# Kernel tuning notes

Hardware: AMD Instinct MI355X
Metric: run time of the kernel (lower is better)

## Reference

```python
import jax, jax.numpy as jnp
import numpy as np

NH = 12   # num_heads
EPS = 1e-6


def _layer_norm(x):
    m = jnp.mean(x, axis=-1, keepdims=True)
    v = jnp.mean((x - m) ** 2, axis=-1, keepdims=True)
    return (x - m) * jax.lax.rsqrt(v + EPS)


def _rms_norm(x, w):
    return x * jax.lax.rsqrt(jnp.mean(x * x, axis=-1, keepdims=True) + EPS) * w


def _rope_cos_sin(f, h, w, head_dim):
    # matches rope_params + calculate_freqs_i: split c=head_dim//2 complex freqs
    # into [c-2*(c//3), c//3, c//3] for the (F,H,W) axes.
    c = head_dim // 2
    inv = 1.0 / (10000.0 ** (np.arange(0, head_dim, 2, dtype=np.float64) / head_dim))
    c1 = c - 2 * (c // 3); c2 = c // 3
    af = np.outer(np.arange(f), inv[:c1])
    ah = np.outer(np.arange(h), inv[c1:c1 + c2])
    aw = np.outer(np.arange(w), inv[c1 + c2:])
    ang = np.concatenate([
        np.broadcast_to(af[:, None, None, :], (f, h, w, c1)),
        np.broadcast_to(ah[None, :, None, :], (f, h, w, c2)),
        np.broadcast_to(aw[None, None, :, :], (f, h, w, c2)),
    ], axis=-1).reshape(f * h * w, c)
    return jnp.asarray(np.cos(ang), jnp.float32), jnp.asarray(np.sin(ang), jnp.float32)


def _apply_rope(x, cos, sin):
    # complex rotation on interleaved pairs; x: [B,L,n,d]
    B, L, n, d = x.shape
    xr = x.reshape(B, L, n, d // 2, 2)
    x0, x1 = xr[..., 0], xr[..., 1]
    co = cos[None, :, None, :]; si = sin[None, :, None, :]
    return jnp.stack([x0 * co - x1 * si, x0 * si + x1 * co], axis=-1).reshape(B, L, n, d)


def _attention(q, k, v):
    scale = 1.0 / jnp.sqrt(jnp.asarray(q.shape[-1], q.dtype))
    s = jnp.einsum('blnd,bmnd->bnlm', q, k) * scale
    return jnp.einsum('bnlm,bmnd->blnd', jax.nn.softmax(s, axis=-1), v)


def _block(x, e, context, mod, sa_wq, sa_bq, sa_wk, sa_bk, sa_wv, sa_bv, sa_wo, sa_bo,
           sa_nq, sa_nk, n3_w, n3_b, ca_wq, ca_bq, ca_wk, ca_bk, ca_wv, ca_bv, ca_wo,
           ca_bo, ca_nq, ca_nk, ffn_w1, ffn_b1, ffn_w2, ffn_b2, f, h, w):
    B, L, C = x.shape
    D = C // NH
    em = mod + e                      # [B,6,C] AdaLN shift/scale/gate params
    cos, sin = _rope_cos_sin(f, h, w, D)
    # --- self-attention with AdaLN modulation + RoPE + qk RMSNorm ---
    xa = _layer_norm(x) * (1.0 + em[:, 1:2]) + em[:, 0:1]
    q = _rms_norm(xa @ sa_wq + sa_bq, sa_nq).reshape(B, L, NH, D)
    k = _rms_norm(xa @ sa_wk + sa_bk, sa_nk).reshape(B, L, NH, D)
    v = (xa @ sa_wv + sa_bv).reshape(B, L, NH, D)
    q = _apply_rope(q, cos, sin)
    k = _apply_rope(k, cos, sin)
    y = _attention(q, k, v).reshape(B, L, C) @ sa_wo + sa_bo
    x = x + y * em[:, 2:3]
    # --- t2v cross-attention (norm3 is affine LayerNorm) ---
    L2 = context.shape[1]
    xc = _layer_norm(x) * n3_w + n3_b
    q = _rms_norm(xc @ ca_wq + ca_bq, ca_nq).reshape(B, L, NH, D)
    k = _rms_norm(context @ ca_wk + ca_bk, ca_nk).reshape(B, L2, NH, D)
    v = (context @ ca_wv + ca_bv).reshape(B, L2, NH, D)
    x = x + (_attention(q, k, v).reshape(B, L, C) @ ca_wo + ca_bo)
    # --- FFN (GELU-tanh) with AdaLN modulation ---
    xf = _layer_norm(x) * (1.0 + em[:, 4:5]) + em[:, 3:4]
    y = jax.nn.gelu(xf @ ffn_w1 + ffn_b1, approximate=True) @ ffn_w2 + ffn_b2
    return x + y * em[:, 5:6]


def setup_inputs() -> dict:
    key = jax.random.key(0)
    ks = jax.random.split(key, 16)
    B, L2, C, FFN = 1, 512, 1536, 8960
    F, H, W = 9, 16, 28
    L = F * H * W  # 4032
    def mk(i, shape, s=0.02):
        return jax.random.normal(ks[i], shape, jnp.float32) * s
    return {
        'x': jax.random.normal(ks[0], (B, L, C), jnp.float32),
        'e': jax.random.normal(ks[1], (B, 6, C), jnp.float32),
        'context': jax.random.normal(ks[2], (B, L2, C), jnp.float32),
        'mod': jax.random.normal(ks[3], (1, 6, C), jnp.float32) / jnp.sqrt(float(C)),
        'sa_wq': mk(4, (C, C)), 'sa_bq': jnp.zeros((C,), jnp.float32),
        'sa_wk': mk(5, (C, C)), 'sa_bk': jnp.zeros((C,), jnp.float32),
        'sa_wv': mk(6, (C, C)), 'sa_bv': jnp.zeros((C,), jnp.float32),
        'sa_wo': mk(7, (C, C)), 'sa_bo': jnp.zeros((C,), jnp.float32),
        'sa_nq': jnp.ones((C,), jnp.float32), 'sa_nk': jnp.ones((C,), jnp.float32),
        'n3_w': jnp.ones((C,), jnp.float32), 'n3_b': jnp.zeros((C,), jnp.float32),
        'ca_wq': mk(8, (C, C)), 'ca_bq': jnp.zeros((C,), jnp.float32),
        'ca_wk': mk(9, (C, C)), 'ca_bk': jnp.zeros((C,), jnp.float32),
        'ca_wv': mk(10, (C, C)), 'ca_bv': jnp.zeros((C,), jnp.float32),
        'ca_wo': mk(11, (C, C)), 'ca_bo': jnp.zeros((C,), jnp.float32),
        'ca_nq': jnp.ones((C,), jnp.float32), 'ca_nk': jnp.ones((C,), jnp.float32),
        'ffn_w1': mk(12, (C, FFN)), 'ffn_b1': jnp.zeros((FFN,), jnp.float32),
        'ffn_w2': mk(13, (FFN, C)), 'ffn_b2': jnp.zeros((C,), jnp.float32),
        'f': F, 'h': H, 'w': W,
    }


def reference(x, e, context, mod, sa_wq, sa_bq, sa_wk, sa_bk, sa_wv, sa_bv, sa_wo,
              sa_bo, sa_nq, sa_nk, n3_w, n3_b, ca_wq, ca_bq, ca_wk, ca_bk, ca_wv,
              ca_bv, ca_wo, ca_bo, ca_nq, ca_nk, ffn_w1, ffn_b1, ffn_w2, ffn_b2,
              f, h, w):
    return _block(x, e, context, mod, sa_wq, sa_bq, sa_wk, sa_bk, sa_wv, sa_bv,
                  sa_wo, sa_bo, sa_nq, sa_nk, n3_w, n3_b, ca_wq, ca_bq, ca_wk,
                  ca_bk, ca_wv, ca_bv, ca_wo, ca_bo, ca_nq, ca_nk, ffn_w1, ffn_b1,
                  ffn_w2, ffn_b2, f, h, w)
```

## Files before the change

kernel.cpp:

```cpp
#include <hip/hip_runtime.h>
#include <math.h>


#define L_SEQ 4032
#define L_PAD 4096
#define C_DIM 1536
#define L_CTX 512
#define FFN_DIM 8960
#define NHEAD 12
#define DHEAD 128

typedef __attribute__((ext_vector_type(8))) short short8;
typedef __attribute__((ext_vector_type(4))) float floatx4;

__device__ inline unsigned short f2bf(float x) {
  unsigned int u = __float_as_uint(x);
  u += 0x7fffu + ((u >> 16) & 1u);
  return (unsigned short)(u >> 16);
}

__device__ inline float2 block_sum2(float2 v) {
  __shared__ float2 red[4];
#pragma unroll
  for (int o = 32; o > 0; o >>= 1) {
    v.x += __shfl_xor(v.x, o, 64);
    v.y += __shfl_xor(v.y, o, 64);
  }
  int wave = threadIdx.x >> 6;
  if ((threadIdx.x & 63) == 0) red[wave] = v;
  __syncthreads();
  float2 t = make_float2(0.f, 0.f);
#pragma unroll
  for (int i = 0; i < 4; ++i) { t.x += red[i].x; t.y += red[i].y; }
  return t;
}

__global__ void add_kernel(float* __restrict__ o, const float* __restrict__ a,
                           const float* __restrict__ b, int n) {
  int i = blockIdx.x * 256 + threadIdx.x;
  if (i < n) o[i] = a[i] + b[i];
}

__global__ void concat3_kernel(float* __restrict__ o, const float* __restrict__ a,
                               const float* __restrict__ b, const float* __restrict__ c) {
  int i = blockIdx.x * 256 + threadIdx.x;
  if (i < C_DIM) {
    o[i] = a[i];
    o[C_DIM + i] = b[i];
    if (c) o[2 * C_DIM + i] = c[i];
  }
}

__global__ void f32_to_bf16_kernel(unsigned short* __restrict__ o,
                                   const float* __restrict__ in, int n) {
  int i = (blockIdx.x * 256 + threadIdx.x) * 4;
  if (i < n) {
    float4 v = *(const float4*)&in[i];
    ushort4 o4 = {f2bf(v.x), f2bf(v.y), f2bf(v.z), f2bf(v.w)};
    *(ushort4*)&o[i] = o4;
  }
}

__global__ __launch_bounds__(256) void transpose_bf16_kernel(
    const float* __restrict__ W, unsigned short* __restrict__ WT, int K, int N) {
  __shared__ float t[32][33];
  int n0 = blockIdx.x * 32, k0 = blockIdx.y * 32;
  int c = threadIdx.x & 31, r0 = threadIdx.x >> 5;
#pragma unroll
  for (int i = 0; i < 4; ++i) {
    int r = r0 + 8 * i;
    t[r][c] = W[(size_t)(k0 + r) * N + n0 + c];
  }
  __syncthreads();
#pragma unroll
  for (int i = 0; i < 4; ++i) {
    int r = r0 + 8 * i;
    WT[(size_t)(n0 + r) * K + k0 + c] = f2bf(t[c][r]);
  }
}

__global__ __launch_bounds__(256) void transpose_v_kernel(
    const float* __restrict__ V, unsigned short* __restrict__ Vt, int stride, int Lk) {
  __shared__ float t[32][33];
  int k0 = blockIdx.x * 32, c0 = blockIdx.y * 32;
  int c = threadIdx.x & 31, r0 = threadIdx.x >> 5;
#pragma unroll
  for (int i = 0; i < 4; ++i) {
    int r = r0 + 8 * i;
    t[r][c] = V[(size_t)(k0 + r) * stride + c0 + c];
  }
  __syncthreads();
#pragma unroll
  for (int i = 0; i < 4; ++i) {
    int r = r0 + 8 * i;
    Vt[(size_t)(c0 + r) * Lk + k0 + c] = f2bf(t[c][r]);
  }
}

__global__ __launch_bounds__(256) void ln_affine_kernel(
    unsigned short* __restrict__ out, const float* __restrict__ in,
    const float* __restrict__ sc, const float* __restrict__ sh, float addOne) {
  int row = blockIdx.x;
  const float* xr = in + (size_t)row * C_DIM;
  float vals[C_DIM / 256];
  float2 p = make_float2(0.f, 0.f);
  int cnt = 0;
  for (int c = threadIdx.x; c < C_DIM; c += 256) {
    float v = xr[c];
    vals[cnt++] = v;
    p.x += v; p.y += v * v;
  }
  float2 t = block_sum2(p);
  float mean = t.x * (1.f / C_DIM);
  float var = t.y * (1.f / C_DIM) - mean * mean;
  float r = rsqrtf(var + 1e-6f);
  cnt = 0;
  for (int c = threadIdx.x; c < C_DIM; c += 256) {
    float xh = (vals[cnt++] - mean) * r;
    out[(size_t)row * C_DIM + c] = f2bf(xh * (addOne + sc[c]) + sh[c]);
  }
}

template <int ROPE>
__global__ __launch_bounds__(256) void rms_post_kernel(
    unsigned short* __restrict__ obf, const float* __restrict__ in,
    const float* __restrict__ w, const float* __restrict__ cosb,
    const float* __restrict__ sinb, int stride) {
  int row = blockIdx.x;
  const float* xr = in + (size_t)row * stride;
  int c0 = threadIdx.x * 6;
  float v[6];
  *(float2*)&v[0] = *(const float2*)&xr[c0];
  *(float2*)&v[2] = *(const float2*)&xr[c0 + 2];
  *(float2*)&v[4] = *(const float2*)&xr[c0 + 4];
  float s2 = 0.f;
#pragma unroll
  for (int i = 0; i < 6; ++i) s2 += v[i] * v[i];
  float2 t = block_sum2(make_float2(s2, 0.f));
  float r = rsqrtf(t.x * (1.f / C_DIM) + 1e-6f);
#pragma unroll
  for (int i = 0; i < 6; ++i) v[i] *= r * w[c0 + i];
  if (ROPE) {
#pragma unroll
    for (int i = 0; i < 3; ++i) {
      int c = c0 + 2 * i;
      int j = (c & 127) >> 1;
      float co = cosb[row * 64 + j], si = sinb[row * 64 + j];
      float a = v[2 * i], b = v[2 * i + 1];
      v[2 * i] = a * co - b * si;
      v[2 * i + 1] = a * si + b * co;
    }
  }
  unsigned short* op = obf + (size_t)row * C_DIM + c0;
  ushort2 o01 = {f2bf(v[0]), f2bf(v[1])};
  ushort2 o23 = {f2bf(v[2]), f2bf(v[3])};
  ushort2 o45 = {f2bf(v[4]), f2bf(v[5])};
  *(ushort2*)&op[0] = o01;
  *(ushort2*)&op[2] = o23;
  *(ushort2*)&op[4] = o45;
}

__global__ void rope_tables_kernel(float* __restrict__ cosb, float* __restrict__ sinb) {
  int l = blockIdx.x, j = threadIdx.x;
  int f = l / (16 * 28);
  int rem = l % (16 * 28);
  int hh = rem / 28, ww = rem % 28;
  double inv = pow(10000.0, -(double)(2 * j) / 128.0);
  double pos = (j < 22) ? (double)f : ((j < 43) ? (double)hh : (double)ww);
  double ang = pos * inv;
  cosb[l * 64 + j] = (float)cos(ang);
  sinb[l * 64 + j] = (float)sin(ang);
}

__device__ inline float gelu_tanh(float x) {
  float x3 = x * x * x;
  return 0.5f * x * (1.f + tanhf(0.79788456080286535588f * (x + 0.044715f * x3)));
}

template <int EPI>
__global__ __launch_bounds__(256) void mgemm_kernel(
    const unsigned short* __restrict__ A, const unsigned short* __restrict__ BT,
    const float* __restrict__ bias, void* __restrict__ Cout,
    const float* __restrict__ resid, const float* __restrict__ gate,
    int N, int K, int Mlimit) {
  __shared__ short sA[2][4096];
  __shared__ short sB[2][4096];
  const int tid = threadIdx.x;
  const int wv = tid >> 6, lane = tid & 63;
  const int lm = lane & 15, lq = lane >> 4;
  const int wr = wv >> 1, wc = wv & 1;

  const int gx = gridDim.x;
  const int nwg = gx * gridDim.y;
  int flat = blockIdx.y * gx + blockIdx.x;
  {
    int qq = nwg >> 3, rr = nwg & 7;
    int xcd = flat & 7, idx = flat >> 3;
    flat = (xcd < rr ? xcd * (qq + 1) : rr * (qq + 1) + (xcd - rr) * qq) + idx;
  }
  const int row0 = (flat / gx) * 128, col0 = (flat % gx) * 128;

  floatx4 zero4 = {0.f, 0.f, 0.f, 0.f};
  floatx4 acc[4][4];
#pragma unroll
  for (int i = 0; i < 4; ++i)
#pragma unroll
    for (int j = 0; j < 4; ++j) acc[i][j] = zero4;

  const unsigned short* Abase = A + ((size_t)row0 + lm) * K + lq * 8;
  const unsigned short* Bbase = BT + ((size_t)col0 + lm) * K + lq * 8;

  auto stage = [&](int buf, int k0) {
#pragma unroll
    for (int t = 0; t < 2; ++t) {
      int g = wv * 2 + t;
      __builtin_amdgcn_global_load_lds(
          (const __attribute__((address_space(1))) void*)(Abase + (size_t)(g * 16) * K + k0),
          (__attribute__((address_space(3))) void*)(sA[buf] + g * 512), 16, 0, 0);
      __builtin_amdgcn_global_load_lds(
          (const __attribute__((address_space(1))) void*)(Bbase + (size_t)(g * 16) * K + k0),
          (__attribute__((address_space(3))) void*)(sB[buf] + g * 512), 16, 0, 0);
    }
  };

  stage(0, 0);
  __syncthreads();
  int cur = 0;
  const int nk = K >> 5;
  for (int t = 0; t < nk; ++t) {
    if (t + 1 < nk) stage(cur ^ 1, (t + 1) << 5);
    const short* sAc = &sA[cur][0];
    const short* sBc = &sB[cur][0];
    short8 af[4], bfv[4];
#pragma unroll
    for (int mt = 0; mt < 4; ++mt)
      af[mt] = *(const short8*)(sAc + (wr * 4 + mt) * 512 + lane * 8);
#pragma unroll
    for (int nt = 0; nt < 4; ++nt)
      bfv[nt] = *(const short8*)(sBc + (wc * 4 + nt) * 512 + lane * 8);
#pragma unroll
    for (int mt = 0; mt < 4; ++mt)
#pragma unroll
      for (int nt = 0; nt < 4; ++nt)
        acc[mt][nt] = __builtin_amdgcn_mfma_f32_16x16x32_bf16(
            af[mt], bfv[nt], acc[mt][nt], 0, 0, 0);
    __syncthreads();
    cur ^= 1;
  }

#pragma unroll
  for (int nt = 0; nt < 4; ++nt) {
    int colg = col0 + wc * 64 + nt * 16 + lm;
    float bv = bias[colg];
    float gv = (EPI == 2 && gate) ? gate[colg] : 1.f;
#pragma unroll
    for (int mt = 0; mt < 4; ++mt) {
#pragma unroll
      for (int r = 0; r < 4; ++r) {
        int rowg = row0 + wr * 64 + mt * 16 + lq * 4 + r;
        if (rowg < Mlimit) {
          float v = acc[mt][nt][r] + bv;
          if (EPI == 1) {
            ((unsigned short*)Cout)[(size_t)rowg * N + colg] = f2bf(gelu_tanh(v));
          } else if (EPI == 2) {
            ((float*)Cout)[(size_t)rowg * N + colg] =
                resid[(size_t)rowg * N + colg] + v * gv;
          } else {
            ((float*)Cout)[(size_t)rowg * N + colg] = v;
          }
        }
      }
    }
  }
}

__global__ __launch_bounds__(256) void attn_mfma_kernel(
    const unsigned short* __restrict__ Qb, const unsigned short* __restrict__ Kb,
    const unsigned short* __restrict__ Vt, unsigned short* __restrict__ O,
    int Lk) {
  __shared__ short sK[2][4096];
  __shared__ short sV[2][4096];
  __shared__ short sP[4][512];
  const int h = blockIdx.y;
  const int q0 = blockIdx.x * 64;
  const int tid = threadIdx.x;
  const int wv = tid >> 6, lane = tid & 63;
  const int lm = lane & 15, lq = lane >> 4;
  const float scale2 = 0.12751649737103347f;

  short8 qf[4];
  {
    const unsigned short* qrow =
        Qb + (size_t)(q0 + wv * 16 + lm) * C_DIM + h * DHEAD + lq * 8;
#pragma unroll
    for (int dc = 0; dc < 4; ++dc) qf[dc] = *(const short8*)(qrow + dc * 32);
  }

  floatx4 zero4 = {0.f, 0.f, 0.f, 0.f};
  floatx4 acc[8];
#pragma unroll
  for (int g = 0; g < 8; ++g) acc[g] = zero4;
  float m[4], l[4];
#pragma unroll
  for (int r = 0; r < 4; ++r) { m[r] = -1e30f; l[r] = 0.f; }

  auto stageKV = [&](int buf, int k0) {
#pragma unroll
    for (int t = 0; t < 2; ++t) {
      int g = wv * 2 + t;
      int nt_ = g >> 2, dc = g & 3;
      const unsigned short* srck =
          Kb + (size_t)(k0 + nt_ * 16 + lm) * C_DIM + h * DHEAD + dc * 32 + lq * 8;
      __builtin_amdgcn_global_load_lds(
          (const __attribute__((address_space(1))) void*)srck,
          (__attribute__((address_space(3))) void*)(sK[buf] + g * 512), 16, 0, 0);
      const unsigned short* srcv =
          Vt + (size_t)(h * DHEAD + g * 16 + lm) * Lk + k0 + lq * 8;
      __builtin_amdgcn_global_load_lds(
          (const __attribute__((address_space(1))) void*)srcv,
          (__attribute__((address_space(3))) void*)(sV[buf] + g * 512), 16, 0, 0);
    }
  };

  stageKV(0, 0);
  __syncthreads();
  int cur = 0;
  const int nsteps = Lk >> 5;
  for (int t = 0; t < nsteps; ++t) {
    if (t + 1 < nsteps) stageKV(cur ^ 1, (t + 1) << 5);
    const short* sKc = &sK[cur][0];
    const short* sVc = &sV[cur][0];

    floatx4 s0 = zero4, s1 = zero4;
#pragma unroll
    for (int dc = 0; dc < 4; ++dc) {
      short8 kf0 = *(const short8*)(sKc + dc * 512 + lane * 8);
      short8 kf1 = *(const short8*)(sKc + (4 + dc) * 512 + lane * 8);
      s0 = __builtin_amdgcn_mfma_f32_16x16x32_bf16(qf[dc], kf0, s0, 0, 0, 0);
      s1 = __builtin_amdgcn_mfma_f32_16x16x32_bf16(qf[dc], kf1, s1, 0, 0, 0);
    }

    float e0[4], e1[4], pm[4];
    bool need = false;
#pragma unroll
    for (int r = 0; r < 4; ++r) {
      e0[r] = s0[r] * scale2;
      e1[r] = s1[r] * scale2;
      float mx = fmaxf(e0[r], e1[r]);
      mx = fmaxf(mx, __shfl_xor(mx, 1));
      mx = fmaxf(mx, __shfl_xor(mx, 2));
      mx = fmaxf(mx, __shfl_xor(mx, 4));
      mx = fmaxf(mx, __shfl_xor(mx, 8));
      pm[r] = mx;
      need = need || (mx > m[r] + 11.5f);
    }
    if (__any((int)need)) {
#pragma unroll
      for (int r = 0; r < 4; ++r) {
        float mn = fmaxf(m[r], pm[r]);
        float al = exp2f(m[r] - mn);
        m[r] = mn;
        l[r] *= al;
#pragma unroll
        for (int g = 0; g < 8; ++g) acc[g][r] *= al;
      }
    }
#pragma unroll
    for (int r = 0; r < 4; ++r) {
      float p0 = exp2f(e0[r] - m[r]);
      float p1 = exp2f(e1[r] - m[r]);
      float rs = p0 + p1;
      rs += __shfl_xor(rs, 1);
      rs += __shfl_xor(rs, 2);
      rs += __shfl_xor(rs, 4);
      rs += __shfl_xor(rs, 8);
      l[r] += rs;
      e0[r] = p0;
      e1[r] = p1;
    }
    {
      int base0 = ((lm >> 3) * 16 + lq * 4) * 8 + (lm & 7);
      int base1 = ((2 + (lm >> 3)) * 16 + lq * 4) * 8 + (lm & 7);
#pragma unroll
      for (int r = 0; r < 4; ++r) {
        sP[wv][base0 + r * 8] = (short)f2bf(e0[r]);
        sP[wv][base1 + r * 8] = (short)f2bf(e1[r]);
      }
    }
    asm volatile("" ::: "memory");
    short8 pa = *(const short8*)(&sP[wv][lane * 8]);
#pragma unroll
    for (int g = 0; g < 8; ++g) {
      short8 vf = *(const short8*)(sVc + g * 512 + lane * 8);
      acc[g] = __builtin_amdgcn_mfma_f32_16x16x32_bf16(pa, vf, acc[g], 0, 0, 0);
    }
    __syncthreads();
    cur ^= 1;
  }

  float invl[4];
#pragma unroll
  for (int r = 0; r < 4; ++r) invl[r] = 1.f / l[r];
  unsigned short* orow =
      O + (size_t)(q0 + wv * 16 + lq * 4) * C_DIM + h * DHEAD + lm;
#pragma unroll
  for (int g = 0; g < 8; ++g) {
#pragma unroll
    for (int r = 0; r < 4; ++r) {
      orow[(size_t)r * C_DIM + g * 16] = f2bf(acc[g][r] * invl[r]);
    }
  }
}

extern "C" void kernel_launch(void* const* d_in, const int* in_sizes, int n_in,
                              void* d_out, int out_size, void* d_ws, size_t ws_size,
                              hipStream_t stream) {
  const float* x     = (const float*)d_in[0];
  const float* e     = (const float*)d_in[1];
  const float* ctx   = (const float*)d_in[2];
  const float* mod   = (const float*)d_in[3];
  const float* sa_wq = (const float*)d_in[4];
  const float* sa_bq = (const float*)d_in[5];
  const float* sa_wk = (const float*)d_in[6];
  const float* sa_bk = (const float*)d_in[7];
  const float* sa_wv = (const float*)d_in[8];
  const float* sa_bv = (const float*)d_in[9];
  const float* sa_wo = (const float*)d_in[10];
  const float* sa_bo = (const float*)d_in[11];
  const float* sa_nq = (const float*)d_in[12];
  const float* sa_nk = (const float*)d_in[13];
  const float* n3_w  = (const float*)d_in[14];
  const float* n3_b  = (const float*)d_in[15];
  const float* ca_wq = (const float*)d_in[16];
  const float* ca_bq = (const float*)d_in[17];
  const float* ca_wk = (const float*)d_in[18];
  const float* ca_bk = (const float*)d_in[19];
  const float* ca_wv = (const float*)d_in[20];
  const float* ca_bv = (const float*)d_in[21];
  const float* ca_wo = (const float*)d_in[22];
  const float* ca_bo = (const float*)d_in[23];
  const float* ca_nq = (const float*)d_in[24];
  const float* ca_nk = (const float*)d_in[25];
  const float* ffn_w1 = (const float*)d_in[26];
  const float* ffn_b1 = (const float*)d_in[27];
  const float* ffn_w2 = (const float*)d_in[28];
  const float* ffn_b2 = (const float*)d_in[29];
  float* out = (float*)d_out;

  char* wsb = (char*)d_ws;
  auto alloc_f = [&](size_t n) { float* p = (float*)wsb; wsb += ((n * 4 + 255) / 256) * 256; return p; };
  auto alloc_h = [&](size_t n) { unsigned short* p = (unsigned short*)wsb; wsb += ((n * 2 + 255) / 256) * 256; return p; };

  float* em   = alloc_f(6 * C_DIM);
  float* cosb = alloc_f(L_SEQ * 64);
  float* sinb = alloc_f(L_SEQ * 64);
  float* qkv  = alloc_f((size_t)L_SEQ * 3 * C_DIM);
  float* x1b  = alloc_f((size_t)L_SEQ * C_DIM);
  unsigned short* act_bf  = alloc_h((size_t)L_PAD * C_DIM);
  unsigned short* ctx_bf  = alloc_h((size_t)L_CTX * C_DIM);
  unsigned short* wtqkv = alloc_h((size_t)3 * C_DIM * C_DIM);
  unsigned short* wto   = alloc_h((size_t)C_DIM * C_DIM);
  unsigned short* wtcq  = alloc_h((size_t)C_DIM * C_DIM);
  unsigned short* wtckv = alloc_h((size_t)2 * C_DIM * C_DIM);
  unsigned short* wtco  = alloc_h((size_t)C_DIM * C_DIM);
  unsigned short* wt1   = alloc_h((size_t)FFN_DIM * C_DIM);
  unsigned short* wt2   = alloc_h((size_t)C_DIM * FFN_DIM);
  float* qkv_bias = alloc_f(3 * C_DIM);
  float* ckv_bias = alloc_f(2 * C_DIM);
  unsigned short* kbf_x = alloc_h((size_t)L_CTX * C_DIM);
  unsigned short* vtx   = alloc_h((size_t)C_DIM * L_CTX);

  unsigned short* qbf_self = (unsigned short*)x1b;
  unsigned short* kbf_self = ((unsigned short*)x1b) + (size_t)L_SEQ * C_DIM;
  unsigned short* vt_self  = (unsigned short*)out;
  unsigned short* qbf_x    = (unsigned short*)out;
  float* crossq = qkv;
  float* ckv    = qkv + (size_t)L_SEQ * C_DIM;
  unsigned short* ffnh_bf = (unsigned short*)qkv;

  dim3 gT(C_DIM / 32, C_DIM / 32);
  dim3 gQKV(3 * C_DIM / 128, L_PAD / 128);
  dim3 gGL(C_DIM / 128, L_PAD / 128);
  dim3 gCKV(2 * C_DIM / 128, L_CTX / 128);
  dim3 gAtt(L_SEQ / 64, NHEAD);

  transpose_bf16_kernel<<<gT, 256, 0, stream>>>(sa_wq, wtqkv, C_DIM, C_DIM);
  transpose_bf16_kernel<<<gT, 256, 0, stream>>>(sa_wk, wtqkv + (size_t)C_DIM * C_DIM, C_DIM, C_DIM);
  transpose_bf16_kernel<<<gT, 256, 0, stream>>>(sa_wv, wtqkv + (size_t)2 * C_DIM * C_DIM, C_DIM, C_DIM);
  transpose_bf16_kernel<<<gT, 256, 0, stream>>>(sa_wo, wto, C_DIM, C_DIM);
  transpose_bf16_kernel<<<gT, 256, 0, stream>>>(ca_wq, wtcq, C_DIM, C_DIM);
  transpose_bf16_kernel<<<gT, 256, 0, stream>>>(ca_wk, wtckv, C_DIM, C_DIM);
  transpose_bf16_kernel<<<gT, 256, 0, stream>>>(ca_wv, wtckv + (size_t)C_DIM * C_DIM, C_DIM, C_DIM);
  transpose_bf16_kernel<<<gT, 256, 0, stream>>>(ca_wo, wtco, C_DIM, C_DIM);
  transpose_bf16_kernel<<<dim3(FFN_DIM / 32, C_DIM / 32), 256, 0, stream>>>(ffn_w1, wt1, C_DIM, FFN_DIM);
  transpose_bf16_kernel<<<dim3(C_DIM / 32, FFN_DIM / 32), 256, 0, stream>>>(ffn_w2, wt2, FFN_DIM, C_DIM);
  f32_to_bf16_kernel<<<(L_CTX * C_DIM) / 1024, 256, 0, stream>>>(ctx_bf, ctx, L_CTX * C_DIM);
  concat3_kernel<<<6, 256, 0, stream>>>(qkv_bias, sa_bq, sa_bk, sa_bv);
  concat3_kernel<<<6, 256, 0, stream>>>(ckv_bias, ca_bk, ca_bv, nullptr);

  add_kernel<<<(6 * C_DIM + 255) / 256, 256, 0, stream>>>(em, e, mod, 6 * C_DIM);
  rope_tables_kernel<<<L_SEQ, 64, 0, stream>>>(cosb, sinb);

  const int nv = L_SEQ * C_DIM;

  ln_affine_kernel<<<L_SEQ, 256, 0, stream>>>(act_bf, x, em + C_DIM, em, 1.f);
  mgemm_kernel<0><<<gQKV, 256, 0, stream>>>(act_bf, wtqkv, qkv_bias, qkv,
                                            nullptr, nullptr, 3 * C_DIM, C_DIM, L_SEQ);
  rms_post_kernel<1><<<L_SEQ, 256, 0, stream>>>(qbf_self, qkv, sa_nq, cosb, sinb, 3 * C_DIM);
  rms_post_kernel<1><<<L_SEQ, 256, 0, stream>>>(kbf_self, qkv + C_DIM, sa_nk, cosb, sinb, 3 * C_DIM);
  transpose_v_kernel<<<dim3(L_SEQ / 32, C_DIM / 32), 256, 0, stream>>>(
      qkv + 2 * C_DIM, vt_self, 3 * C_DIM, L_SEQ);
  attn_mfma_kernel<<<gAtt, 256, 0, stream>>>(qbf_self, kbf_self, vt_self, act_bf, L_SEQ);
  mgemm_kernel<2><<<gGL, 256, 0, stream>>>(act_bf, wto, sa_bo, x1b,
                                           x, em + 2 * C_DIM, C_DIM, C_DIM, L_SEQ);

  ln_affine_kernel<<<L_SEQ, 256, 0, stream>>>(act_bf, x1b, n3_w, n3_b, 0.f);
  mgemm_kernel<0><<<gGL, 256, 0, stream>>>(act_bf, wtcq, ca_bq, crossq,
                                           nullptr, nullptr, C_DIM, C_DIM, L_SEQ);
  rms_post_kernel<0><<<L_SEQ, 256, 0, stream>>>(qbf_x, crossq, ca_nq, cosb, sinb, C_DIM);
  mgemm_kernel<0><<<gCKV, 256, 0, stream>>>(ctx_bf, wtckv, ckv_bias, ckv,
                                            nullptr, nullptr, 2 * C_DIM, C_DIM, L_CTX);
  rms_post_kernel<0><<<L_CTX, 256, 0, stream>>>(kbf_x, ckv, ca_nk, cosb, sinb, 2 * C_DIM);
  transpose_v_kernel<<<dim3(L_CTX / 32, C_DIM / 32), 256, 0, stream>>>(
      ckv + C_DIM, vtx, 2 * C_DIM, L_CTX);
  attn_mfma_kernel<<<gAtt, 256, 0, stream>>>(qbf_x, kbf_x, vtx, act_bf, L_CTX);
  mgemm_kernel<2><<<gGL, 256, 0, stream>>>(act_bf, wtco, ca_bo, out,
                                           x1b, nullptr, C_DIM, C_DIM, L_SEQ);

  ln_affine_kernel<<<L_SEQ, 256, 0, stream>>>(act_bf, out, em + 4 * C_DIM, em + 3 * C_DIM, 1.f);
  dim3 g1(FFN_DIM / 128, L_PAD / 128);
  mgemm_kernel<1><<<g1, 256, 0, stream>>>(act_bf, wt1, ffn_b1, ffnh_bf,
                                          nullptr, nullptr, FFN_DIM, C_DIM, L_SEQ);
  dim3 g2(C_DIM / 128, L_PAD / 128);
  mgemm_kernel<2><<<g2, 256, 0, stream>>>(ffnh_bf, wt2, ffn_b2, out,
                                          out, em + 5 * C_DIM, C_DIM, FFN_DIM, L_SEQ);
  (void)nv;
}
```

Measured before the change: 1.647 ms.

## Triple-buffer GEMM loads, transpose attention QK^T, fold softmax scale into Q

The GEMM moves from double to triple LDS buffering with explicit vmcnt waits and raw s_barrier, so two K-tiles are in flight and one barrier is removed per iteration. Attention computes S^T (K as the A operand), so each lane owns a single query row. Row max and row sum then need only two cross-lane shuffles, and P is written to LDS with vector stores. The softmax scale (including log2e) is folded into the Q RMSNorm output, removing a multiply per score. The cost is more LDS per GEMM block, which may lower occupancy, plus rounding changes from pre-scaling Q in bf16.

```diff
diff --git a/kernel.cpp b/kernel.cpp
--- a/kernel.cpp
+++ b/kernel.cpp
@@ -125,7 +125,7 @@
 __global__ __launch_bounds__(256) void rms_post_kernel(
     unsigned short* __restrict__ obf, const float* __restrict__ in,
     const float* __restrict__ w, const float* __restrict__ cosb,
-    const float* __restrict__ sinb, int stride) {
+    const float* __restrict__ sinb, int stride, float ps) {
   int row = blockIdx.x;
   const float* xr = in + (size_t)row * stride;
   int c0 = threadIdx.x * 6;
@@ -137,7 +137,7 @@
 #pragma unroll
   for (int i = 0; i < 6; ++i) s2 += v[i] * v[i];
   float2 t = block_sum2(make_float2(s2, 0.f));
-  float r = rsqrtf(t.x * (1.f / C_DIM) + 1e-6f);
+  float r = rsqrtf(t.x * (1.f / C_DIM) + 1e-6f) * ps;
 #pragma unroll
   for (int i = 0; i < 6; ++i) v[i] *= r * w[c0 + i];
   if (ROPE) {
@@ -183,8 +183,8 @@
     const float* __restrict__ bias, void* __restrict__ Cout,
     const float* __restrict__ resid, const float* __restrict__ gate,
     int N, int K, int Mlimit) {
-  __shared__ short sA[2][4096];
-  __shared__ short sB[2][4096];
+  __shared__ short sA[3][4096];
+  __shared__ short sB[3][4096];
   const int tid = threadIdx.x;
   const int wv = tid >> 6, lane = tid & 63;
   const int lm = lane & 15, lq = lane >> 4;
@@ -224,11 +224,17 @@
   };
 
   stage(0, 0);
-  __syncthreads();
+  stage(1, 32);
+  asm volatile("s_waitcnt vmcnt(4)" ::: "memory");
+  __builtin_amdgcn_s_barrier();
+  __builtin_amdgcn_sched_barrier(0);
+
   int cur = 0;
   const int nk = K >> 5;
   for (int t = 0; t < nk; ++t) {
-    if (t + 1 < nk) stage(cur ^ 1, (t + 1) << 5);
+    int b2 = cur + 2; if (b2 >= 3) b2 -= 3;
+    const bool more = (t + 2 < nk);
+    if (more) stage(b2, (t + 2) << 5);
     const short* sAc = &sA[cur][0];
     const short* sBc = &sB[cur][0];
     short8 af[4], bfv[4];
@@ -244,8 +250,12 @@
       for (int nt = 0; nt < 4; ++nt)
         acc[mt][nt] = __builtin_amdgcn_mfma_f32_16x16x32_bf16(
             af[mt], bfv[nt], acc[mt][nt], 0, 0, 0);
-    __syncthreads();
-    cur ^= 1;
+    __builtin_amdgcn_sched_barrier(0);
+    if (more) { asm volatile("s_waitcnt vmcnt(4)" ::: "memory"); }
+    else      { asm volatile("s_waitcnt vmcnt(0)" ::: "memory"); }
+    __builtin_amdgcn_s_barrier();
+    __builtin_amdgcn_sched_barrier(0);
+    cur = (cur + 1 == 3) ? 0 : cur + 1;
   }
 
 #pragma unroll
@@ -286,7 +296,6 @@
   const int tid = threadIdx.x;
   const int wv = tid >> 6, lane = tid & 63;
   const int lm = lane & 15, lq = lane >> 4;
-  const float scale2 = 0.12751649737103347f;
 
   short8 qf[4];
   {
@@ -300,9 +309,7 @@
   floatx4 acc[8];
 #pragma unroll
   for (int g = 0; g < 8; ++g) acc[g] = zero4;
-  float m[4], l[4];
-#pragma unroll
-  for (int r = 0; r < 4; ++r) { m[r] = -1e30f; l[r] = 0.f; }
+  float m = -1e30f, l = 0.f;
 
   auto stageKV = [&](int buf, int k0) {
 #pragma unroll
@@ -336,56 +343,49 @@
     for (int dc = 0; dc < 4; ++dc) {
       short8 kf0 = *(const short8*)(sKc + dc * 512 + lane * 8);
       short8 kf1 = *(const short8*)(sKc + (4 + dc) * 512 + lane * 8);
-      s0 = __builtin_amdgcn_mfma_f32_16x16x32_bf16(qf[dc], kf0, s0, 0, 0, 0);
-      s1 = __builtin_amdgcn_mfma_f32_16x16x32_bf16(qf[dc], kf1, s1, 0, 0, 0);
-    }
-
-    float e0[4], e1[4], pm[4];
-    bool need = false;
+      s0 = __builtin_amdgcn_mfma_f32_16x16x32_bf16(kf0, qf[dc], s0, 0, 0, 0);
+      s1 = __builtin_amdgcn_mfma_f32_16x16x32_bf16(kf1, qf[dc], s1, 0, 0, 0);
+    }
+
+    float mx = fmaxf(fmaxf(fmaxf(s0[0], s0[1]), fmaxf(s0[2], s0[3])),
+                     fmaxf(fmaxf(s1[0], s1[1]), fmaxf(s1[2], s1[3])));
+    mx = fmaxf(mx, __shfl_xor(mx, 16));
+    mx = fmaxf(mx, __shfl_xor(mx, 32));
+    bool need = mx > m + 11.5f;
+    if (__any((int)need)) {
+      float mn = fmaxf(m, mx);
+      float al = exp2f(m - mn);
+      m = mn;
+      l *= al;
+      float ar[4];
+#pragma unroll
+      for (int r = 0; r < 4; ++r) ar[r] = __shfl(al, lq * 4 + r);
+#pragma unroll
+      for (int g = 0; g < 8; ++g)
+#pragma unroll
+        for (int r = 0; r < 4; ++r) acc[g][r] *= ar[r];
+    }
+    float rs = 0.f;
+    ushort4 pk0, pk1;
 #pragma unroll
     for (int r = 0; r < 4; ++r) {
-      e0[r] = s0[r] * scale2;
-      e1[r] = s1[r] * scale2;
-      float mx = fmaxf(e0[r], e1[r]);
-      mx = fmaxf(mx, __shfl_xor(mx, 1));
-      mx = fmaxf(mx, __shfl_xor(mx, 2));
-      mx = fmaxf(mx, __shfl_xor(mx, 4));
-      mx = fmaxf(mx, __shfl_xor(mx, 8));
-      pm[r] = mx;
-      need = need || (mx > m[r] + 11.5f);
-    }
-    if (__any((int)need)) {
-#pragma unroll
-      for (int r = 0; r < 4; ++r) {
-        float mn = fmaxf(m[r], pm[r]);
-        float al = exp2f(m[r] - mn);
-        m[r] = mn;
-        l[r] *= al;
-#pragma unroll
-        for (int g = 0; g < 8; ++g) acc[g][r] *= al;
-      }
+      float p = exp2f(s0[r] - m);
+      rs += p;
+      ((unsigned short*)&pk0)[r] = f2bf(p);
     }
 #pragma unroll
     for (int r = 0; r < 4; ++r) {
-      float p0 = exp2f(e0[r] - m[r]);
-      float p1 = exp2f(e1[r] - m[r]);
-      float rs = p0 + p1;
-      rs += __shfl_xor(rs, 1);
-      rs += __shfl_xor(rs, 2);
-      rs += __shfl_xor(rs, 4);
-      rs += __shfl_xor(rs, 8);
-      l[r] += rs;
-      e0[r] = p0;
-      e1[r] = p1;
-    }
+      float p = exp2f(s1[r] - m);
+      rs += p;
+      ((unsigned short*)&pk1)[r] = f2bf(p);
+    }
+    rs += __shfl_xor(rs, 16);
+    rs += __shfl_xor(rs, 32);
+    l += rs;
     {
-      int base0 = ((lm >> 3) * 16 + lq * 4) * 8 + (lm & 7);
-      int base1 = ((2 + (lm >> 3)) * 16 + lq * 4) * 8 + (lm & 7);
-#pragma unroll
-      for (int r = 0; r < 4; ++r) {
-        sP[wv][base0 + r * 8] = (short)f2bf(e0[r]);
-        sP[wv][base1 + r * 8] = (short)f2bf(e1[r]);
-      }
+      int baseq = (((lq >> 1) * 16 + lm) << 3) + ((lq & 1) << 2);
+      *(ushort4*)&sP[wv][baseq] = pk0;
+      *(ushort4*)&sP[wv][baseq + 256] = pk1;
     }
     asm volatile("" ::: "memory");
     short8 pa = *(const short8*)(&sP[wv][lane * 8]);
@@ -400,7 +400,7 @@
 
   float invl[4];
 #pragma unroll
-  for (int r = 0; r < 4; ++r) invl[r] = 1.f / l[r];
+  for (int r = 0; r < 4; ++r) invl[r] = 1.f / __shfl(l, lq * 4 + r);
   unsigned short* orow =
       O + (size_t)(q0 + wv * 16 + lq * 4) * C_DIM + h * DHEAD + lm;
 #pragma unroll
@@ -478,6 +478,8 @@
   float* ckv    = qkv + (size_t)L_SEQ * C_DIM;
   unsigned short* ffnh_bf = (unsigned short*)qkv;
 
+  const float qscale = 0.12751649737103347f;
+
   dim3 gT(C_DIM / 32, C_DIM / 32);
   dim3 gQKV(3 * C_DIM / 128, L_PAD / 128);
   dim3 gGL(C_DIM / 128, L_PAD / 128);
@@ -501,13 +503,13 @@
   add_kernel<<<(6 * C_DIM + 255) / 256, 256, 0, stream>>>(em, e, mod, 6 * C_DIM);
   rope_tables_kernel<<<L_SEQ, 64, 0, stream>>>(cosb, sinb);
 
-  const int nv = L_SEQ * C_DIM;
-
   ln_affine_kernel<<<L_SEQ, 256, 0, stream>>>(act_bf, x, em + C_DIM, em, 1.f);
   mgemm_kernel<0><<<gQKV, 256, 0, stream>>>(act_bf, wtqkv, qkv_bias, qkv,
                                             nullptr, nullptr, 3 * C_DIM, C_DIM, L_SEQ);
-  rms_post_kernel<1><<<L_SEQ, 256, 0, stream>>>(qbf_self, qkv, sa_nq, cosb, sinb, 3 * C_DIM);
-  rms_post_kernel<1><<<L_SEQ, 256, 0, stream>>>(kbf_self, qkv + C_DIM, sa_nk, cosb, sinb, 3 * C_DIM);
+  rms_post_kernel<1><<<L_SEQ, 256, 0, stream>>>(qbf_self, qkv, sa_nq, cosb, sinb,
+                                                3 * C_DIM, qscale);
+  rms_post_kernel<1><<<L_SEQ, 256, 0, stream>>>(kbf_self, qkv + C_DIM, sa_nk, cosb, sinb,
+                                                3 * C_DIM, 1.f);
   transpose_v_kernel<<<dim3(L_SEQ / 32, C_DIM / 32), 256, 0, stream>>>(
       qkv + 2 * C_DIM, vt_self, 3 * C_DIM, L_SEQ);
   attn_mfma_kernel<<<gAtt, 256, 0, stream>>>(qbf_self, kbf_self, vt_self, act_bf, L_SEQ);
@@ -517,10 +519,12 @@
   ln_affine_kernel<<<L_SEQ, 256, 0, stream>>>(act_bf, x1b, n3_w, n3_b, 0.f);
   mgemm_kernel<0><<<gGL, 256, 0, stream>>>(act_bf, wtcq, ca_bq, crossq,
                                            nullptr, nullptr, C_DIM, C_DIM, L_SEQ);
-  rms_post_kernel<0><<<L_SEQ, 256, 0, stream>>>(qbf_x, crossq, ca_nq, cosb, sinb, C_DIM);
+  rms_post_kernel<0><<<L_SEQ, 256, 0, stream>>>(qbf_x, crossq, ca_nq, cosb, sinb,
+                                                C_DIM, qscale);
   mgemm_kernel<0><<<gCKV, 256, 0, stream>>>(ctx_bf, wtckv, ckv_bias, ckv,
                                             nullptr, nullptr, 2 * C_DIM, C_DIM, L_CTX);
-  rms_post_kernel<0><<<L_CTX, 256, 0, stream>>>(kbf_x, ckv, ca_nk, cosb, sinb, 2 * C_DIM);
+  rms_post_kernel<0><<<L_CTX, 256, 0, stream>>>(kbf_x, ckv, ca_nk, cosb, sinb,
+                                                2 * C_DIM, 1.f);
   transpose_v_kernel<<<dim3(L_CTX / 32, C_DIM / 32), 256, 0, stream>>>(
       ckv + C_DIM, vtx, 2 * C_DIM, L_CTX);
   attn_mfma_kernel<<<gAtt, 256, 0, stream>>>(qbf_x, kbf_x, vtx, act_bf, L_CTX);
@@ -534,5 +538,4 @@
   dim3 g2(C_DIM / 128, L_PAD / 128);
   mgemm_kernel<2><<<g2, 256, 0, stream>>>(ffnh_bf, wt2, ffn_b2, out,
                                           out, em + 5 * C_DIM, C_DIM, FFN_DIM, L_SEQ);
-  (void)nv;
-}
+}
```

After: 1.564 ms. 1.05x faster.
